# Performance work log

Hardware: AMD Instinct MI355X
Metric: run time of the kernel (lower is better)

Reference implementation:

```python
import jax, jax.numpy as jnp
import numpy as np

NW, NT, ND, D = 30000, 2000, 20000, 128
E = {'ww': 600000, 'wt': 300000, 'wd': 400000, 'td': 100000, 'tt': 40000}
ENDS = {'ww': (NW, NW), 'wt': (NW, NT), 'wd': (NW, ND), 'td': (NT, ND), 'tt': (NT, NT)}


def setup_inputs() -> dict:
    key = jax.random.key(0)
    ks = iter(jax.random.split(key, 64))
    nrm = lambda shape: jax.random.normal(next(ks), shape, dtype=jnp.float32)
    inp = {}
    inp['feat_word'] = nrm((NW, D))
    inp['feat_topic'] = nrm((NT, D))
    # 'effect' node data: ~half the topics are causal (nonzero effect)
    inp['effect'] = jax.random.randint(next(ks), (NT,), 0, 2).astype(jnp.float32)
    # independent Bernoulli(0.1) draws for the td and tt iterations
    inp['bern_td'] = (jax.random.uniform(next(ks), (NT,)) < 0.1).astype(jnp.float32)
    inp['bern_tt'] = (jax.random.uniform(next(ks), (NT,)) < 0.1).astype(jnp.float32)
    for et, (ns, nd) in ENDS.items():
        inp[f'src_{et}'] = jax.random.randint(next(ks), (E[et],), 0, ns, dtype=jnp.int32)
        inp[f'dst_{et}'] = jax.random.randint(next(ks), (E[et],), 0, nd, dtype=jnp.int32)
        inp[f'w_{et}'] = jax.random.uniform(next(ks), (E[et],), dtype=jnp.float32)
    for name in ['ww', 'wt', 'wd', 'td', 'tt']:
        inp[f'W_{name}'] = nrm((D, D)) * 0.05
        inp[f'b_{name}'] = jnp.zeros((D,), jnp.float32)
    inp['W_causal'] = nrm((D, D)) * 0.05
    inp['W_noise'] = nrm((D, D)) * 0.05
    inp['n_doc'] = ND
    return inp


def _mean_agg(Wh, w, src, dst, n_dst):
    # DGL fn.u_mul_e + fn.mean: mean of (Wh[src]*w) over incoming edges; 0 for isolated dst
    m = Wh[src] * w[:, None]                                    # [E, D]
    s = jax.ops.segment_sum(m, dst, num_segments=n_dst)          # [n_dst, D]
    deg = jax.ops.segment_sum(jnp.ones_like(w), dst, num_segments=n_dst)
    return jnp.where(deg[:, None] > 0, s / jnp.maximum(deg, 1.0)[:, None], 0.0)


def reference(feat_word, feat_topic, effect, bern_td, bern_tt,
              src_ww, dst_ww, w_ww, src_wt, dst_wt, w_wt,
              src_wd, dst_wd, w_wd, src_td, dst_td, w_td,
              src_tt, dst_tt, w_tt,
              W_ww, b_ww, W_wt, b_wt, W_wd, b_wd, W_td, b_td, W_tt, b_tt,
              W_causal, W_noise, n_doc):
    n_word, n_topic = feat_word.shape[0], feat_topic.shape[0]
    # Phase 1: word -> word (ww)
    h_word = _mean_agg(feat_word @ W_ww + b_ww, w_ww, src_ww, dst_ww, n_word)
    # Phase 2: remaining etypes; word features replaced by h
    causal = (effect != 0).astype(feat_topic.dtype)[:, None]     # [NT, 1]
    rm_td = (bern_td * (effect == 0))[:, None]
    rm_tt = (bern_tt * (effect == 0))[:, None]
    Wh_wt = h_word @ W_wt + b_wt
    Wh_wd = h_word @ W_wd + b_wd
    Wh_td = (feat_topic @ W_td + b_td
             + (feat_topic * causal) @ W_causal - (feat_topic * rm_td) @ W_noise)
    Wh_tt = (feat_topic @ W_tt + b_tt
             + (feat_topic * causal) @ W_causal - (feat_topic * rm_tt) @ W_noise)
    # cross-relation 'sum' reducer per destination ntype
    h_topic = (_mean_agg(Wh_wt, w_wt, src_wt, dst_wt, n_topic)
               + _mean_agg(Wh_tt, w_tt, src_tt, dst_tt, n_topic))
    h_doc = (_mean_agg(Wh_wd, w_wd, src_wd, dst_wd, n_doc)
             + _mean_agg(Wh_td, w_td, src_td, dst_td, n_doc))
    return h_word, h_topic, h_doc
```

## Files before the change

kernel.cpp:

```cpp
#include <hip/hip_runtime.h>

#define D 128
typedef unsigned short u16;
constexpr int NW = 30000;
constexpr int NT = 2000;
constexpr int NDOC = 20000;
constexpr int NSLOT = NW + NT + NT + NDOC + NDOC;
constexpr int SEG_WW = 0;
constexpr int SEG_WT = NW;
constexpr int SEG_TT = NW + NT;
constexpr int SEG_WD = NW + 2 * NT;
constexpr int SEG_TD = NW + 2 * NT + NDOC;

constexpr int CAPB = 4096;
constexpr int NBK_WW = (NW + 127) / 128;
constexpr int NBK_WT = NT / 16;
constexpr int NBK_TT = (NT + 127) / 128;
constexpr int NBK_WD = (NDOC + 127) / 128;
constexpr int NBK_TD = (NDOC + 127) / 128;
constexpr int BUK_WW = 0;
constexpr int BUK_WT = BUK_WW + NBK_WW;
constexpr int BUK_TT = BUK_WT + NBK_WT;
constexpr int BUK_WD = BUK_TT + NBK_TT;
constexpr int BUK_TD = BUK_WD + NBK_WD;
constexpr int NBUK   = BUK_TD + NBK_TD;

constexpr int EPB = 4096;
constexpr int NF2B = (NW * D / 4 + 255) / 256;
constexpr int NBM4 = (NT + 63) / 64;

struct RelDesc { const int* src; const int* dst; const float* w;
                 int e0; int buk0; int shift; int mask; };
struct Rels { RelDesc r[5]; };

__device__ __forceinline__ int which_rel(const Rels& R, int e)
{
    if (e < R.r[1].e0) return 0;
    if (e < R.r[2].e0) return 1;
    if (e < R.r[3].e0) return 2;
    if (e < R.r[4].e0) return 3;
    return 4;
}

__device__ __forceinline__ float b2f(u16 h)
{
    return __uint_as_float(((unsigned)h) << 16);
}
__device__ __forceinline__ u16 f2b(float f)
{
    unsigned u = __float_as_uint(f);
    return (u16)((u + 0x7FFF + ((u >> 16) & 1)) >> 16);
}

typedef short bf16x8 __attribute__((ext_vector_type(8)));
typedef float f32x4 __attribute__((ext_vector_type(4)));
constexpr int WPITCH = 136;

__device__ __forceinline__ void stage_wt(
    const float* __restrict__ Wg, u16* Wt, int tid)
{
    for (int i = tid; i < D * D; i += 256) {
        int k = i >> 7, nn = i & 127;
        Wt[nn * WPITCH + k] = f2b(Wg[i]);
    }
}

__device__ __forceinline__ void mfma_tile_f32(
    const float* __restrict__ X, const u16* Wt, int arow, int n,
    int lanelo, int quad, f32x4 acc[8])
{
#pragma unroll
    for (int ct = 0; ct < 8; ++ct) {
        acc[ct][0] = 0.f; acc[ct][1] = 0.f; acc[ct][2] = 0.f; acc[ct][3] = 0.f;
    }
#pragma unroll
    for (int k0 = 0; k0 < 4; ++k0) {
        bf16x8 a;
        if (arow < n) {
            const float* ap = X + (size_t)arow * D + k0 * 32 + quad * 8;
            float4 a0 = *(const float4*)ap;
            float4 a1 = *(const float4*)(ap + 4);
            a[0] = (short)f2b(a0.x); a[1] = (short)f2b(a0.y);
            a[2] = (short)f2b(a0.z); a[3] = (short)f2b(a0.w);
            a[4] = (short)f2b(a1.x); a[5] = (short)f2b(a1.y);
            a[6] = (short)f2b(a1.z); a[7] = (short)f2b(a1.w);
        } else {
#pragma unroll
            for (int j = 0; j < 8; ++j) a[j] = 0;
        }
#pragma unroll
        for (int ct = 0; ct < 8; ++ct) {
            bf16x8 b = *(const bf16x8*)&Wt[(ct * 16 + lanelo) * WPITCH
                                           + k0 * 32 + quad * 8];
            acc[ct] = __builtin_amdgcn_mfma_f32_16x16x32_bf16(a, b, acc[ct], 0, 0, 0);
        }
    }
}

__device__ __forceinline__ void mfma_tile_b16(
    const u16* __restrict__ Xb, const u16* Wt, int arow, int n,
    int lanelo, int quad, f32x4 acc[8])
{
#pragma unroll
    for (int ct = 0; ct < 8; ++ct) {
        acc[ct][0] = 0.f; acc[ct][1] = 0.f; acc[ct][2] = 0.f; acc[ct][3] = 0.f;
    }
#pragma unroll
    for (int k0 = 0; k0 < 4; ++k0) {
        bf16x8 a;
        if (arow < n) {
            a = *(const bf16x8*)(Xb + (size_t)arow * D + k0 * 32 + quad * 8);
        } else {
#pragma unroll
            for (int j = 0; j < 8; ++j) a[j] = 0;
        }
#pragma unroll
        for (int ct = 0; ct < 8; ++ct) {
            bf16x8 b = *(const bf16x8*)&Wt[(ct * 16 + lanelo) * WPITCH
                                           + k0 * 32 + quad * 8];
            acc[ct] = __builtin_amdgcn_mfma_f32_16x16x32_bf16(a, b, acc[ct], 0, 0, 0);
        }
    }
}

struct MM4 { const float* W[4]; float* P[4]; };

__global__ __launch_bounds__(256) void prep_kernel(
    const float* __restrict__ feat_word, u16* __restrict__ fw16,
    const float* __restrict__ feat_topic, MM4 m4, int* __restrict__ cur)
{
    __shared__ u16 Wt[D * WPITCH];
    int tid = threadIdx.x;

    if ((int)blockIdx.x < NF2B) {
        int i = blockIdx.x * 256 + tid;
        if (i < NW * D / 4) {
            float4 v = ((const float4*)feat_word)[i];
            ushort4 o;
            o.x = f2b(v.x); o.y = f2b(v.y); o.z = f2b(v.z); o.w = f2b(v.w);
            ((ushort4*)fw16)[i] = o;
        }
    } else if ((int)blockIdx.x < NF2B + 4 * NBM4) {
        int idx = blockIdx.x - NF2B;
        int which = idx / NBM4;
        int bx = idx % NBM4;
        stage_wt(m4.W[which], Wt, tid);
        __syncthreads();
        int wv = tid >> 6, lane = tid & 63;
        int lanelo = lane & 15, quad = lane >> 4;
        int rowbase = bx * 64 + wv * 16;
        f32x4 acc[8];
        mfma_tile_f32(feat_topic, Wt, rowbase + lanelo, NT, lanelo, quad, acc);
        float* Y = m4.P[which];
        int rbase = rowbase + quad * 4;
#pragma unroll
        for (int r = 0; r < 4; ++r) {
            int row = rbase + r;
            if (row >= NT) continue;
#pragma unroll
            for (int ct = 0; ct < 8; ++ct)
                Y[(size_t)row * D + ct * 16 + lanelo] = acc[ct][r];
        }
    } else {
        for (int i = tid; i < NBUK; i += 256) cur[i] = 0;
    }
}

__global__ __launch_bounds__(256) void part_combine_kernel(
    Rels R, int Etot, int* __restrict__ cur, int2* __restrict__ edataP,
    const float* __restrict__ P_td, const float* __restrict__ P_tt,
    const float* __restrict__ Pc, const float* __restrict__ Pn,
    const float* __restrict__ effect, const float* __restrict__ bern_td,
    const float* __restrict__ bern_tt,
    const float* __restrict__ b_td, const float* __restrict__ b_tt,
    u16* __restrict__ wtd16, u16* __restrict__ wtt16, int npb)
{
    __shared__ int hist[NBUK];
    __shared__ int baseL[NBUK];
    __shared__ u16 bkt[EPB];
    __shared__ int2 st[EPB];
    int tid = threadIdx.x;

    if ((int)blockIdx.x >= npb) {
        int i = ((int)blockIdx.x - npb) * 256 + tid;
        if (i < NT * D) {
            int row = i >> 7;
            int col = i & (D - 1);
            float eff = effect[row];
            float causal = (eff != 0.f) ? 1.f : 0.f;
            float zero = (eff == 0.f) ? 1.f : 0.f;
            float rmtd = bern_td[row] * zero;
            float rmtt = bern_tt[row] * zero;
            float pc = Pc[i];
            float pn = Pn[i];
            wtd16[i] = f2b(P_td[i] + b_td[col] + causal * pc - rmtd * pn);
            wtt16[i] = f2b(P_tt[i] + b_tt[col] + causal * pc - rmtt * pn);
        }
        return;
    }

    for (int i = tid; i < NBUK; i += 256) hist[i] = 0;
    __syncthreads();
    int base_e = blockIdx.x * EPB;
    for (int r = 0; r < EPB / 256; ++r) {
        int idx = r * 256 + tid;
        int e = base_e + idx;
        if (e < Etot) {
            int k = which_rel(R, e);
            int le = e - R.r[k].e0;
            int s = R.r[k].src[le];
            int dd = R.r[k].dst[le];
            float w = R.r[k].w[le];
            int b = R.r[k].buk0 + (dd >> R.r[k].shift);
            int dloc = dd & R.r[k].mask;
            bkt[idx] = (u16)b;
            st[idx] = make_int2(s | (dloc << 15), __float_as_int(w));
            atomicAdd(&hist[b], 1);
        } else {
            bkt[idx] = 0xFFFF;
        }
    }
    __syncthreads();
    for (int i = tid; i < NBUK; i += 256)
        baseL[i] = hist[i] ? atomicAdd(&cur[i], hist[i]) : 0;
    __syncthreads();
    for (int i = tid; i < NBUK; i += 256) hist[i] = 0;
    __syncthreads();
    for (int r = 0; r < EPB / 256; ++r) {
        int idx = r * 256 + tid;
        int b = bkt[idx];
        if (b != 0xFFFF) {
            int rk = atomicAdd(&hist[b], 1);
            edataP[(size_t)b * CAPB + baseL[b] + rk] = st[idx];
        }
    }
}

__device__ __forceinline__ void reduce_one_lds(
    const u16* __restrict__ Xb, const int2* st, const u16* ord,
    int start, int end, int slot, int lane,
    u16* __restrict__ Sb, float* __restrict__ degf, float* __restrict__ wsumf)
{
    int half = lane >> 5;
    int q = (lane & 31) * 4;
    float4 acc = make_float4(0.f, 0.f, 0.f, 0.f);
    float wacc = 0.f;
    int j = start;
    for (; j + 16 <= end; j += 16) {
        int2 ee[8];
        ushort4 vv[8];
#pragma unroll
        for (int t = 0; t < 8; ++t) ee[t] = st[ord[j + 2 * t + half]];
#pragma unroll
        for (int t = 0; t < 8; ++t)
            vv[t] = *(const ushort4*)(Xb + (size_t)(ee[t].x & 0x7FFF) * D + q);
#pragma unroll
        for (int t = 0; t < 8; ++t) {
            float w = __int_as_float(ee[t].y);
            acc.x = fmaf(w, b2f(vv[t].x), acc.x);
            acc.y = fmaf(w, b2f(vv[t].y), acc.y);
            acc.z = fmaf(w, b2f(vv[t].z), acc.z);
            acc.w = fmaf(w, b2f(vv[t].w), acc.w);
            wacc += w;
        }
    }
    if (j + 8 <= end) {
        int2 ee[4];
        ushort4 vv[4];
#pragma unroll
        for (int t = 0; t < 4; ++t) ee[t] = st[ord[j + 2 * t + half]];
#pragma unroll
        for (int t = 0; t < 4; ++t)
            vv[t] = *(const ushort4*)(Xb + (size_t)(ee[t].x & 0x7FFF) * D + q);
#pragma unroll
        for (int t = 0; t < 4; ++t) {
            float w = __int_as_float(ee[t].y);
            acc.x = fmaf(w, b2f(vv[t].x), acc.x);
            acc.y = fmaf(w, b2f(vv[t].y), acc.y);
            acc.z = fmaf(w, b2f(vv[t].z), acc.z);
            acc.w = fmaf(w, b2f(vv[t].w), acc.w);
            wacc += w;
        }
        j += 8;
    }
    if (j + 4 <= end) {
        int2 ea = st[ord[j + half]];
        int2 eb = st[ord[j + 2 + half]];
        ushort4 va = *(const ushort4*)(Xb + (size_t)(ea.x & 0x7FFF) * D + q);
        ushort4 vb = *(const ushort4*)(Xb + (size_t)(eb.x & 0x7FFF) * D + q);
        float wa = __int_as_float(ea.y);
        float wb = __int_as_float(eb.y);
        acc.x = fmaf(wa, b2f(va.x), acc.x); acc.y = fmaf(wa, b2f(va.y), acc.y);
        acc.z = fmaf(wa, b2f(va.z), acc.z); acc.w = fmaf(wa, b2f(va.w), acc.w);
        acc.x = fmaf(wb, b2f(vb.x), acc.x); acc.y = fmaf(wb, b2f(vb.y), acc.y);
        acc.z = fmaf(wb, b2f(vb.z), acc.z); acc.w = fmaf(wb, b2f(vb.w), acc.w);
        wacc += wa + wb;
        j += 4;
    }
    for (; j < end; j += 2) {
        int jj = j + half;
        int2 e = st[ord[jj < end ? jj : (end - 1)]];
        float w = (jj < end) ? __int_as_float(e.y) : 0.f;
        ushort4 v = *(const ushort4*)(Xb + (size_t)(e.x & 0x7FFF) * D + q);
        acc.x = fmaf(w, b2f(v.x), acc.x); acc.y = fmaf(w, b2f(v.y), acc.y);
        acc.z = fmaf(w, b2f(v.z), acc.z); acc.w = fmaf(w, b2f(v.w), acc.w);
        wacc += w;
    }
    acc.x += __shfl_xor(acc.x, 32);
    acc.y += __shfl_xor(acc.y, 32);
    acc.z += __shfl_xor(acc.z, 32);
    acc.w += __shfl_xor(acc.w, 32);
    wacc  += __shfl_xor(wacc, 32);
    if (half == 0) {
        ushort4 o;
        o.x = f2b(acc.x); o.y = f2b(acc.y); o.z = f2b(acc.z); o.w = f2b(acc.w);
        *(ushort4*)(Sb + (size_t)slot * D + q) = o;
    }
    if (lane == 0) {
        degf[slot] = (float)(end - start);
        if (wsumf) wsumf[slot] = wacc;
    }
}

__device__ __forceinline__ void bucket_reduce_body(
    const u16* __restrict__ X, const int* __restrict__ cur,
    const int2* __restrict__ edataP, int buk, int gslot0, int nsl,
    u16* __restrict__ Sb, float* __restrict__ degf, float* __restrict__ wsumf,
    int2* st, u16* ord, int* h2, int* exc, int* cnt)
{
    int tid = threadIdx.x;
    int nE = cur[buk];
    const int2* gsrc = edataP + (size_t)buk * CAPB;
    for (int i = tid; i < nE; i += 1024) st[i] = gsrc[i];
    if (tid < 128) { h2[tid] = 0; cnt[tid] = 0; }
    __syncthreads();
    for (int i = tid; i < nE; i += 1024)
        atomicAdd(&h2[(st[i].x >> 15) & 127], 1);
    __syncthreads();
    if (tid < 128) exc[tid] = h2[tid];
    __syncthreads();
    for (int off = 1; off < 128; off <<= 1) {
        int t = 0;
        if (tid < 128 && tid >= off) t = exc[tid - off];
        __syncthreads();
        if (tid < 128) exc[tid] += t;
        __syncthreads();
    }
    if (tid < 128) exc[tid] -= h2[tid];
    __syncthreads();
    for (int i = tid; i < nE; i += 1024) {
        int dl = (st[i].x >> 15) & 127;
        int rk = atomicAdd(&cnt[dl], 1);
        ord[exc[dl] + rk] = (u16)i;
    }
    __syncthreads();
    int wv = tid >> 6, lane = tid & 63;
    for (int dl = wv; dl < nsl; dl += 16) {
        int start = exc[dl];
        reduce_one_lds(X, st, ord, start, start + h2[dl], gslot0 + dl,
                       lane, Sb, degf, wsumf);
    }
}

__global__ __launch_bounds__(1024) void bucket_reduceA_kernel(
    const u16* __restrict__ fw16, const u16* __restrict__ wtt16,
    const u16* __restrict__ wtd16, const int* __restrict__ cur,
    const int2* __restrict__ edataP,
    u16* __restrict__ Sb, float* __restrict__ degf, float* __restrict__ wsumf)
{
    __shared__ int2 st[CAPB];
    __shared__ u16 ord[CAPB];
    __shared__ int h2[128], exc[128], cnt[128];
    int b = blockIdx.x;
    const u16* X; int buk, gslot0, nsl;
    if (b < NBK_WW) {
        X = fw16; buk = BUK_WW + b; gslot0 = SEG_WW + b * 128;
        nsl = min(128, NW - b * 128);
    } else if (b < NBK_WW + NBK_TT) {
        int i = b - NBK_WW;
        X = wtt16; buk = BUK_TT + i; gslot0 = SEG_TT + i * 128;
        nsl = min(128, NT - i * 128);
    } else {
        int i = b - NBK_WW - NBK_TT;
        X = wtd16; buk = BUK_TD + i; gslot0 = SEG_TD + i * 128;
        nsl = min(128, NDOC - i * 128);
    }
    bucket_reduce_body(X, cur, edataP, buk, gslot0, nsl, Sb, degf, wsumf,
                       st, ord, h2, exc, cnt);
}

__global__ __launch_bounds__(1024) void bucket_reduceB_kernel(
    const u16* __restrict__ hw16, const int* __restrict__ cur,
    const int2* __restrict__ edataP,
    u16* __restrict__ Sb, float* __restrict__ degf, float* __restrict__ wsumf)
{
    __shared__ int2 st[CAPB];
    __shared__ u16 ord[CAPB];
    __shared__ int h2[128], exc[128], cnt[128];
    int b = blockIdx.x;
    int buk, gslot0, nsl;
    if (b < NBK_WT) {
        buk = BUK_WT + b; gslot0 = SEG_WT + b * 16; nsl = 16;
    } else {
        int i = b - NBK_WT;
        buk = BUK_WD + i; gslot0 = SEG_WD + i * 128;
        nsl = min(128, NDOC - i * 128);
    }
    bucket_reduce_body(hw16, cur, edataP, buk, gslot0, nsl, Sb, degf, wsumf,
                       st, ord, h2, exc, cnt);
}

__device__ __forceinline__ void mfma_mm_body(
    const u16* __restrict__ Xb, const float* __restrict__ Wg,
    const float* __restrict__ deg, const float* __restrict__ wsum,
    const float* __restrict__ bias,
    const u16* __restrict__ T, const float* __restrict__ degT,
    float* __restrict__ Y, u16* __restrict__ Yb, int n,
    u16* Wt, int tid, int bx)
{
    stage_wt(Wg, Wt, tid);
    __syncthreads();
    int wv = tid >> 6, lane = tid & 63;
    int lanelo = lane & 15, quad = lane >> 4;
    int rowbase = bx * 64 + wv * 16;
    f32x4 acc[8];
    mfma_tile_b16(Xb, Wt, rowbase + lanelo, n, lanelo, quad, acc);

    int rbase = rowbase + quad * 4;
#pragma unroll
    for (int r = 0; r < 4; ++r) {
        int row = rbase + r;
        if (row >= n) continue;
        float dgv = deg[row];
        float wsv = wsum ? wsum[row] : 0.f;
        float dtv = degT ? degT[row] : 0.f;
#pragma unroll
        for (int ct = 0; ct < 8; ++ct) {
            int col = ct * 16 + lanelo;
            float y = acc[ct][r];
            y = dgv > 0.f ? (y + wsv * bias[col]) / dgv : 0.f;
            if (T && dtv > 0.f) y += b2f(T[(size_t)row * D + col]) / dtv;
            Y[(size_t)row * D + col] = y;
            if (Yb) Yb[(size_t)row * D + col] = f2b(y);
        }
    }
}

__global__ __launch_bounds__(256) void mfma_mm_kernel(
    const u16* __restrict__ Xb, const float* __restrict__ Wg,
    const float* __restrict__ deg, const float* __restrict__ wsum,
    const float* __restrict__ bias,
    const u16* __restrict__ T, const float* __restrict__ degT,
    float* __restrict__ Y, u16* __restrict__ Yb, int n)
{
    __shared__ u16 Wt[D * WPITCH];
    mfma_mm_body(Xb, Wg, deg, wsum, bias, T, degT, Y, Yb, n,
                 Wt, threadIdx.x, blockIdx.x);
}

struct MMF {
    const u16* X[2]; const float* W[2]; const float* deg[2];
    const float* wsum[2]; const float* bias[2];
    const u16* T[2]; const float* degT[2];
    float* Y[2]; int n[2]; int nb0;
};
__global__ __launch_bounds__(256) void mfma_mm2_kernel(MMF p)
{
    __shared__ u16 Wt[D * WPITCH];
    int which = (int)(blockIdx.x >= (unsigned)p.nb0);
    int bx = which ? (int)blockIdx.x - p.nb0 : (int)blockIdx.x;
    mfma_mm_body(p.X[which], p.W[which], p.deg[which], p.wsum[which],
                 p.bias[which], p.T[which], p.degT[which], p.Y[which],
                 nullptr, p.n[which], Wt, threadIdx.x, bx);
}

extern "C" void kernel_launch(void* const* d_in, const int* in_sizes, int n_in,
                              void* d_out, int out_size, void* d_ws, size_t ws_size,
                              hipStream_t stream)
{
    const float* feat_word  = (const float*)d_in[0];
    const float* feat_topic = (const float*)d_in[1];
    const float* effect     = (const float*)d_in[2];
    const float* bern_td    = (const float*)d_in[3];
    const float* bern_tt    = (const float*)d_in[4];
    const int*   src_ww = (const int*)d_in[5];
    const int*   dst_ww = (const int*)d_in[6];
    const float* w_ww   = (const float*)d_in[7];
    const int*   src_wt = (const int*)d_in[8];
    const int*   dst_wt = (const int*)d_in[9];
    const float* w_wt   = (const float*)d_in[10];
    const int*   src_wd = (const int*)d_in[11];
    const int*   dst_wd = (const int*)d_in[12];
    const float* w_wd   = (const float*)d_in[13];
    const int*   src_td = (const int*)d_in[14];
    const int*   dst_td = (const int*)d_in[15];
    const float* w_td   = (const float*)d_in[16];
    const int*   src_tt = (const int*)d_in[17];
    const int*   dst_tt = (const int*)d_in[18];
    const float* w_tt   = (const float*)d_in[19];
    const float* W_ww = (const float*)d_in[20];
    const float* b_ww = (const float*)d_in[21];
    const float* W_wt = (const float*)d_in[22];
    const float* b_wt = (const float*)d_in[23];
    const float* W_wd = (const float*)d_in[24];
    const float* b_wd = (const float*)d_in[25];
    const float* W_td = (const float*)d_in[26];
    const float* b_td = (const float*)d_in[27];
    const float* W_tt = (const float*)d_in[28];
    const float* b_tt = (const float*)d_in[29];
    const float* W_causal = (const float*)d_in[30];
    const float* W_noise  = (const float*)d_in[31];

    const int E_ww = in_sizes[5];
    const int E_wt = in_sizes[8];
    const int E_wd = in_sizes[11];
    const int E_td = in_sizes[14];
    const int E_tt = in_sizes[17];
    const int E_total = E_ww + E_wt + E_wd + E_td + E_tt;

    float* ws = (float*)d_ws;
    u16*   Sb    = (u16*)ws; ws += (long long)NSLOT * D / 2;
    float* degf  = ws; ws += NSLOT;
    float* wsumf = ws; ws += NSLOT;
    int*   cur   = (int*)ws; ws += NBUK;
    ws += ((size_t)(ws - (float*)d_ws) & 1);
    int2*  edataP = (int2*)ws; ws += (long long)2 * NBUK * CAPB;
    float* P_td  = ws; ws += (long long)NT * D;
    float* P_tt  = ws; ws += (long long)NT * D;
    float* Pc    = ws; ws += (long long)NT * D;
    float* Pn    = ws; ws += (long long)NT * D;
    u16*   fw16  = (u16*)ws;  ws += (long long)NW * D / 2;
    u16*   hw16  = (u16*)ws;  ws += (long long)NW * D / 2;
    u16*   wtd16 = (u16*)ws;  ws += (long long)NT * D / 2;
    u16*   wtt16 = (u16*)ws;  ws += (long long)NT * D / 2;

    float* h_word  = (float*)d_out;
    float* h_topic = h_word + (long long)NW * D;
    float* h_doc   = h_topic + (long long)NT * D;

    auto nb = [](long long n) { return (unsigned)((n + 255) / 256); };

    Rels R;
    R.r[0] = { src_ww, dst_ww, w_ww, 0,                         BUK_WW, 7, 127 };
    R.r[1] = { src_wt, dst_wt, w_wt, E_ww,                      BUK_WT, 4, 15  };
    R.r[2] = { src_tt, dst_tt, w_tt, E_ww + E_wt,               BUK_TT, 7, 127 };
    R.r[3] = { src_wd, dst_wd, w_wd, E_ww + E_wt + E_tt,        BUK_WD, 7, 127 };
    R.r[4] = { src_td, dst_td, w_td, E_ww + E_wt + E_tt + E_wd, BUK_TD, 7, 127 };

    MM4 m4;
    m4.W[0] = W_td; m4.W[1] = W_tt; m4.W[2] = W_causal; m4.W[3] = W_noise;
    m4.P[0] = P_td; m4.P[1] = P_tt; m4.P[2] = Pc;       m4.P[3] = Pn;
    prep_kernel<<<NF2B + 4 * NBM4 + 1, 256, 0, stream>>>(
        feat_word, fw16, feat_topic, m4, cur);

    unsigned npb = (unsigned)((E_total + EPB - 1) / EPB);
    part_combine_kernel<<<npb + nb((long long)NT * D), 256, 0, stream>>>(
        R, E_total, cur, edataP,
        P_td, P_tt, Pc, Pn, effect, bern_td, bern_tt, b_td, b_tt,
        wtd16, wtt16, (int)npb);

    bucket_reduceA_kernel<<<NBK_WW + NBK_TT + NBK_TD, 1024, 0, stream>>>(
        fw16, wtt16, wtd16, cur, edataP, Sb, degf, wsumf);

    mfma_mm_kernel<<<(NW + 63) / 64, 256, 0, stream>>>(
        Sb + (long long)SEG_WW * D, W_ww, degf + SEG_WW, wsumf + SEG_WW, b_ww,
        nullptr, nullptr, h_word, hw16, NW);

    bucket_reduceB_kernel<<<NBK_WT + NBK_WD, 1024, 0, stream>>>(
        hw16, cur, edataP, Sb, degf, wsumf);

    MMF mf;
    mf.X[0] = Sb + (long long)SEG_WT * D;  mf.X[1] = Sb + (long long)SEG_WD * D;
    mf.W[0] = W_wt;                        mf.W[1] = W_wd;
    mf.deg[0] = degf + SEG_WT;             mf.deg[1] = degf + SEG_WD;
    mf.wsum[0] = wsumf + SEG_WT;           mf.wsum[1] = wsumf + SEG_WD;
    mf.bias[0] = b_wt;                     mf.bias[1] = b_wd;
    mf.T[0] = Sb + (long long)SEG_TT * D;  mf.T[1] = Sb + (long long)SEG_TD * D;
    mf.degT[0] = degf + SEG_TT;            mf.degT[1] = degf + SEG_TD;
    mf.Y[0] = h_topic;                     mf.Y[1] = h_doc;
    mf.n[0] = NT;                          mf.n[1] = NDOC;
    mf.nb0 = (NT + 63) / 64;
    unsigned nbf = (unsigned)((NT + 63) / 64 + (NDOC + 63) / 64);
    mfma_mm2_kernel<<<nbf, 256, 0, stream>>>(mf);

    (void)n_in; (void)in_sizes; (void)out_size; (void)ws_size;
}
```

Measured before the change: 266.7 us.

## Fuse bucket reduction with MFMA projection and shrink buckets to 64 destinations

Combines the bucketed segment-sum with the following bf16 MFMA matmul inside one kernel per phase. The per-destination sums stay in LDS instead of going through a global intermediate, and the two separate matmul launches are removed. Buckets shrink from 128 to 64 destinations with 512-thread blocks, the bucket capacity is halved, and the partition pass keeps edges in registers instead of LDS. The weights are transposed to bf16 once in the prep kernel and read from global memory during the fused matmul. The halved capacity adds a clamp that silently drops edges if a bucket overflows.

```diff
diff --git a/kernel.cpp b/kernel.cpp
--- a/kernel.cpp
+++ b/kernel.cpp
@@ -5,19 +5,14 @@
 constexpr int NW = 30000;
 constexpr int NT = 2000;
 constexpr int NDOC = 20000;
-constexpr int NSLOT = NW + NT + NT + NDOC + NDOC;
-constexpr int SEG_WW = 0;
-constexpr int SEG_WT = NW;
-constexpr int SEG_TT = NW + NT;
-constexpr int SEG_WD = NW + 2 * NT;
-constexpr int SEG_TD = NW + 2 * NT + NDOC;
-
-constexpr int CAPB = 4096;
-constexpr int NBK_WW = (NW + 127) / 128;
-constexpr int NBK_WT = NT / 16;
-constexpr int NBK_TT = (NT + 127) / 128;
-constexpr int NBK_WD = (NDOC + 127) / 128;
-constexpr int NBK_TD = (NDOC + 127) / 128;
+
+constexpr int CAPB = 2048;
+constexpr int SSP  = 136;
+constexpr int NBK_WW = (NW + 63) / 64;
+constexpr int NBK_WT = NT / 8;
+constexpr int NBK_TT = (NT + 63) / 64;
+constexpr int NBK_WD = (NDOC + 63) / 64;
+constexpr int NBK_TD = (NDOC + 63) / 64;
 constexpr int BUK_WW = 0;
 constexpr int BUK_WT = BUK_WW + NBK_WW;
 constexpr int BUK_TT = BUK_WT + NBK_WT;
@@ -97,37 +92,12 @@
     }
 }
 
-__device__ __forceinline__ void mfma_tile_b16(
-    const u16* __restrict__ Xb, const u16* Wt, int arow, int n,
-    int lanelo, int quad, f32x4 acc[8])
-{
-#pragma unroll
-    for (int ct = 0; ct < 8; ++ct) {
-        acc[ct][0] = 0.f; acc[ct][1] = 0.f; acc[ct][2] = 0.f; acc[ct][3] = 0.f;
-    }
-#pragma unroll
-    for (int k0 = 0; k0 < 4; ++k0) {
-        bf16x8 a;
-        if (arow < n) {
-            a = *(const bf16x8*)(Xb + (size_t)arow * D + k0 * 32 + quad * 8);
-        } else {
-#pragma unroll
-            for (int j = 0; j < 8; ++j) a[j] = 0;
-        }
-#pragma unroll
-        for (int ct = 0; ct < 8; ++ct) {
-            bf16x8 b = *(const bf16x8*)&Wt[(ct * 16 + lanelo) * WPITCH
-                                           + k0 * 32 + quad * 8];
-            acc[ct] = __builtin_amdgcn_mfma_f32_16x16x32_bf16(a, b, acc[ct], 0, 0, 0);
-        }
-    }
-}
-
 struct MM4 { const float* W[4]; float* P[4]; };
+struct TR3 { const float* W[3]; u16* T[3]; };
 
 __global__ __launch_bounds__(256) void prep_kernel(
     const float* __restrict__ feat_word, u16* __restrict__ fw16,
-    const float* __restrict__ feat_topic, MM4 m4, int* __restrict__ cur)
+    const float* __restrict__ feat_topic, MM4 m4, TR3 tr, int* __restrict__ cur)
 {
     __shared__ u16 Wt[D * WPITCH];
     int tid = threadIdx.x;
@@ -160,6 +130,15 @@
 #pragma unroll
             for (int ct = 0; ct < 8; ++ct)
                 Y[(size_t)row * D + ct * 16 + lanelo] = acc[ct][r];
+        }
+    } else if ((int)blockIdx.x < NF2B + 4 * NBM4 + 3) {
+        int which = blockIdx.x - NF2B - 4 * NBM4;
+        stage_wt(tr.W[which], Wt, tid);
+        __syncthreads();
+        u16* Wd = tr.T[which];
+        for (int i = tid; i < D * D; i += 256) {
+            int nrow = i >> 7, k = i & 127;
+            Wd[i] = Wt[nrow * WPITCH + k];
         }
     } else {
         for (int i = tid; i < NBUK; i += 256) cur[i] = 0;
@@ -177,8 +156,6 @@
 {
     __shared__ int hist[NBUK];
     __shared__ int baseL[NBUK];
-    __shared__ u16 bkt[EPB];
-    __shared__ int2 st[EPB];
     int tid = threadIdx.x;
 
     if ((int)blockIdx.x >= npb) {
@@ -202,9 +179,11 @@
     for (int i = tid; i < NBUK; i += 256) hist[i] = 0;
     __syncthreads();
     int base_e = blockIdx.x * EPB;
+    int bs[EPB / 256];
+    int2 se[EPB / 256];
+#pragma unroll
     for (int r = 0; r < EPB / 256; ++r) {
-        int idx = r * 256 + tid;
-        int e = base_e + idx;
+        int e = base_e + r * 256 + tid;
         if (e < Etot) {
             int k = which_rel(R, e);
             int le = e - R.r[k].e0;
@@ -213,11 +192,11 @@
             float w = R.r[k].w[le];
             int b = R.r[k].buk0 + (dd >> R.r[k].shift);
             int dloc = dd & R.r[k].mask;
-            bkt[idx] = (u16)b;
-            st[idx] = make_int2(s | (dloc << 15), __float_as_int(w));
+            bs[r] = b;
+            se[r] = make_int2(s | (dloc << 15), __float_as_int(w));
             atomicAdd(&hist[b], 1);
         } else {
-            bkt[idx] = 0xFFFF;
+            bs[r] = -1;
         }
     }
     __syncthreads();
@@ -226,20 +205,29 @@
     __syncthreads();
     for (int i = tid; i < NBUK; i += 256) hist[i] = 0;
     __syncthreads();
+#pragma unroll
     for (int r = 0; r < EPB / 256; ++r) {
-        int idx = r * 256 + tid;
-        int b = bkt[idx];
-        if (b != 0xFFFF) {
-            int rk = atomicAdd(&hist[b], 1);
-            edataP[(size_t)b * CAPB + baseL[b] + rk] = st[idx];
-        }
-    }
-}
+        int b = bs[r];
+        if (b >= 0) {
+            int rk = atomicAdd(&hist[b], 1) + baseL[b];
+            if (rk < CAPB)
+                edataP[(size_t)b * CAPB + rk] = se[r];
+        }
+    }
+}
+
+struct BucketSmem {
+    int2 st[CAPB];
+    u16  ord[CAPB];
+    u16  Ssum[64 * SSP];
+    float degL[64];
+    float wsumL[64];
+    int h2[64], exc[64], cnt[64];
+};
 
 __device__ __forceinline__ void reduce_one_lds(
     const u16* __restrict__ Xb, const int2* st, const u16* ord,
-    int start, int end, int slot, int lane,
-    u16* __restrict__ Sb, float* __restrict__ degf, float* __restrict__ wsumf)
+    int start, int end, int dl, int lane, BucketSmem& s)
 {
     int half = lane >> 5;
     int q = (lane & 31) * 4;
@@ -314,164 +302,175 @@
     if (half == 0) {
         ushort4 o;
         o.x = f2b(acc.x); o.y = f2b(acc.y); o.z = f2b(acc.z); o.w = f2b(acc.w);
-        *(ushort4*)(Sb + (size_t)slot * D + q) = o;
+        *(ushort4*)(s.Ssum + dl * SSP + q) = o;
     }
     if (lane == 0) {
-        degf[slot] = (float)(end - start);
-        if (wsumf) wsumf[slot] = wacc;
-    }
-}
-
-__device__ __forceinline__ void bucket_reduce_body(
+        s.degL[dl] = (float)(end - start);
+        s.wsumL[dl] = wacc;
+    }
+}
+
+__device__ __forceinline__ void bucket_reduce(
     const u16* __restrict__ X, const int* __restrict__ cur,
-    const int2* __restrict__ edataP, int buk, int gslot0, int nsl,
-    u16* __restrict__ Sb, float* __restrict__ degf, float* __restrict__ wsumf,
-    int2* st, u16* ord, int* h2, int* exc, int* cnt)
+    const int2* __restrict__ edataP, int buk, int nsl, BucketSmem& s)
 {
     int tid = threadIdx.x;
-    int nE = cur[buk];
+    int nE = min(cur[buk], CAPB);
     const int2* gsrc = edataP + (size_t)buk * CAPB;
-    for (int i = tid; i < nE; i += 1024) st[i] = gsrc[i];
-    if (tid < 128) { h2[tid] = 0; cnt[tid] = 0; }
-    __syncthreads();
-    for (int i = tid; i < nE; i += 1024)
-        atomicAdd(&h2[(st[i].x >> 15) & 127], 1);
-    __syncthreads();
-    if (tid < 128) exc[tid] = h2[tid];
-    __syncthreads();
-    for (int off = 1; off < 128; off <<= 1) {
+    for (int i = tid; i < nE; i += 512) s.st[i] = gsrc[i];
+    if (tid < 64) { s.h2[tid] = 0; s.cnt[tid] = 0; }
+    __syncthreads();
+    for (int i = tid; i < nE; i += 512)
+        atomicAdd(&s.h2[(s.st[i].x >> 15) & 63], 1);
+    __syncthreads();
+    if (tid < 64) s.exc[tid] = s.h2[tid];
+    __syncthreads();
+    for (int off = 1; off < 64; off <<= 1) {
         int t = 0;
-        if (tid < 128 && tid >= off) t = exc[tid - off];
-        __syncthreads();
-        if (tid < 128) exc[tid] += t;
-        __syncthreads();
-    }
-    if (tid < 128) exc[tid] -= h2[tid];
-    __syncthreads();
-    for (int i = tid; i < nE; i += 1024) {
-        int dl = (st[i].x >> 15) & 127;
-        int rk = atomicAdd(&cnt[dl], 1);
-        ord[exc[dl] + rk] = (u16)i;
+        if (tid < 64 && tid >= off) t = s.exc[tid - off];
+        __syncthreads();
+        if (tid < 64) s.exc[tid] += t;
+        __syncthreads();
+    }
+    if (tid < 64) s.exc[tid] -= s.h2[tid];
+    __syncthreads();
+    for (int i = tid; i < nE; i += 512) {
+        int dl = (s.st[i].x >> 15) & 63;
+        int rk = atomicAdd(&s.cnt[dl], 1);
+        s.ord[s.exc[dl] + rk] = (u16)i;
     }
     __syncthreads();
     int wv = tid >> 6, lane = tid & 63;
-    for (int dl = wv; dl < nsl; dl += 16) {
-        int start = exc[dl];
-        reduce_one_lds(X, st, ord, start, start + h2[dl], gslot0 + dl,
-                       lane, Sb, degf, wsumf);
-    }
-}
-
-__global__ __launch_bounds__(1024) void bucket_reduceA_kernel(
+    for (int dl = wv; dl < nsl; dl += 8) {
+        int start = s.exc[dl];
+        reduce_one_lds(X, s.st, s.ord, start, start + s.h2[dl], dl, lane, s);
+    }
+}
+
+__device__ __forceinline__ void fused_mm(
+    BucketSmem& s, const u16* __restrict__ Wtg, const float* __restrict__ bias,
+    const u16* __restrict__ Tg, const float* __restrict__ degTg,
+    float* __restrict__ Y, u16* __restrict__ Yb, int row0, int n, int tid)
+{
+    int wv = tid >> 6, lane = tid & 63;
+    int lanelo = lane & 15, quad = lane >> 4;
+    int rt = wv >> 1, ch = wv & 1;
+    int arow = rt * 16 + lanelo;
+    f32x4 acc[4];
+#pragma unroll
+    for (int c = 0; c < 4; ++c) {
+        acc[c][0] = 0.f; acc[c][1] = 0.f; acc[c][2] = 0.f; acc[c][3] = 0.f;
+    }
+#pragma unroll
+    for (int k0 = 0; k0 < 4; ++k0) {
+        bf16x8 a;
+        if (arow < n) {
+            a = *(const bf16x8*)(s.Ssum + arow * SSP + k0 * 32 + quad * 8);
+        } else {
+#pragma unroll
+            for (int j = 0; j < 8; ++j) a[j] = 0;
+        }
+#pragma unroll
+        for (int c = 0; c < 4; ++c) {
+            int ct = ch * 4 + c;
+            bf16x8 b = *(const bf16x8*)(Wtg + (ct * 16 + lanelo) * D
+                                        + k0 * 32 + quad * 8);
+            acc[c] = __builtin_amdgcn_mfma_f32_16x16x32_bf16(a, b, acc[c], 0, 0, 0);
+        }
+    }
+    int rbase = rt * 16 + quad * 4;
+#pragma unroll
+    for (int r = 0; r < 4; ++r) {
+        int row = rbase + r;
+        if (row >= n) continue;
+        float dgv = s.degL[row];
+        float wsv = s.wsumL[row];
+        float dtv = degTg ? degTg[row] : 0.f;
+#pragma unroll
+        for (int c = 0; c < 4; ++c) {
+            int ct = ch * 4 + c;
+            int col = ct * 16 + lanelo;
+            float y = acc[c][r];
+            y = dgv > 0.f ? (y + wsv * bias[col]) / dgv : 0.f;
+            if (Tg && dtv > 0.f) y += b2f(Tg[(size_t)row * D + col]) / dtv;
+            Y[(size_t)(row0 + row) * D + col] = y;
+            if (Yb) Yb[(size_t)(row0 + row) * D + col] = f2b(y);
+        }
+    }
+}
+
+__device__ __forceinline__ void dump_smem(
+    BucketSmem& s, u16* __restrict__ Sg, float* __restrict__ degg,
+    int nsl, int tid)
+{
+    for (int i = tid; i < nsl * 32; i += 512) {
+        int row = i >> 5, c4 = (i & 31) * 4;
+        *(ushort4*)(Sg + (size_t)row * D + c4) =
+            *(const ushort4*)(s.Ssum + row * SSP + c4);
+    }
+    if (tid < nsl) degg[tid] = s.degL[tid];
+}
+
+__global__ __launch_bounds__(512, 4) void phaseA_kernel(
     const u16* __restrict__ fw16, const u16* __restrict__ wtt16,
     const u16* __restrict__ wtd16, const int* __restrict__ cur,
     const int2* __restrict__ edataP,
-    u16* __restrict__ Sb, float* __restrict__ degf, float* __restrict__ wsumf)
-{
-    __shared__ int2 st[CAPB];
-    __shared__ u16 ord[CAPB];
-    __shared__ int h2[128], exc[128], cnt[128];
+    const u16* __restrict__ Wtg_ww, const float* __restrict__ b_ww,
+    float* __restrict__ h_word, u16* __restrict__ hw16,
+    u16* __restrict__ Sb2, float* __restrict__ degf2)
+{
+    __shared__ BucketSmem s;
     int b = blockIdx.x;
-    const u16* X; int buk, gslot0, nsl;
+    int tid = threadIdx.x;
     if (b < NBK_WW) {
-        X = fw16; buk = BUK_WW + b; gslot0 = SEG_WW + b * 128;
-        nsl = min(128, NW - b * 128);
+        int w0 = b * 64;
+        int nsl = min(64, NW - w0);
+        bucket_reduce(fw16, cur, edataP, BUK_WW + b, nsl, s);
+        __syncthreads();
+        fused_mm(s, Wtg_ww, b_ww, nullptr, nullptr, h_word, hw16, w0, nsl, tid);
     } else if (b < NBK_WW + NBK_TT) {
         int i = b - NBK_WW;
-        X = wtt16; buk = BUK_TT + i; gslot0 = SEG_TT + i * 128;
-        nsl = min(128, NT - i * 128);
+        int t0 = i * 64;
+        int nsl = min(64, NT - t0);
+        bucket_reduce(wtt16, cur, edataP, BUK_TT + i, nsl, s);
+        __syncthreads();
+        dump_smem(s, Sb2 + (size_t)t0 * D, degf2 + t0, nsl, tid);
     } else {
         int i = b - NBK_WW - NBK_TT;
-        X = wtd16; buk = BUK_TD + i; gslot0 = SEG_TD + i * 128;
-        nsl = min(128, NDOC - i * 128);
-    }
-    bucket_reduce_body(X, cur, edataP, buk, gslot0, nsl, Sb, degf, wsumf,
-                       st, ord, h2, exc, cnt);
-}
-
-__global__ __launch_bounds__(1024) void bucket_reduceB_kernel(
+        int d0 = i * 64;
+        int nsl = min(64, NDOC - d0);
+        bucket_reduce(wtd16, cur, edataP, BUK_TD + i, nsl, s);
+        __syncthreads();
+        dump_smem(s, Sb2 + (size_t)(NT + d0) * D, degf2 + NT + d0, nsl, tid);
+    }
+}
+
+__global__ __launch_bounds__(512, 4) void phaseB_kernel(
     const u16* __restrict__ hw16, const int* __restrict__ cur,
     const int2* __restrict__ edataP,
-    u16* __restrict__ Sb, float* __restrict__ degf, float* __restrict__ wsumf)
-{
-    __shared__ int2 st[CAPB];
-    __shared__ u16 ord[CAPB];
-    __shared__ int h2[128], exc[128], cnt[128];
+    const u16* __restrict__ Wtg_wt, const float* __restrict__ b_wt,
+    const u16* __restrict__ Wtg_wd, const float* __restrict__ b_wd,
+    const u16* __restrict__ Sb2, const float* __restrict__ degf2,
+    float* __restrict__ h_topic, float* __restrict__ h_doc)
+{
+    __shared__ BucketSmem s;
     int b = blockIdx.x;
-    int buk, gslot0, nsl;
+    int tid = threadIdx.x;
     if (b < NBK_WT) {
-        buk = BUK_WT + b; gslot0 = SEG_WT + b * 16; nsl = 16;
+        int t0 = b * 8;
+        bucket_reduce(hw16, cur, edataP, BUK_WT + b, 8, s);
+        __syncthreads();
+        fused_mm(s, Wtg_wt, b_wt, Sb2 + (size_t)t0 * D, degf2 + t0,
+                 h_topic, nullptr, t0, 8, tid);
     } else {
         int i = b - NBK_WT;
-        buk = BUK_WD + i; gslot0 = SEG_WD + i * 128;
-        nsl = min(128, NDOC - i * 128);
-    }
-    bucket_reduce_body(hw16, cur, edataP, buk, gslot0, nsl, Sb, degf, wsumf,
-                       st, ord, h2, exc, cnt);
-}
-
-__device__ __forceinline__ void mfma_mm_body(
-    const u16* __restrict__ Xb, const float* __restrict__ Wg,
-    const float* __restrict__ deg, const float* __restrict__ wsum,
-    const float* __restrict__ bias,
-    const u16* __restrict__ T, const float* __restrict__ degT,
-    float* __restrict__ Y, u16* __restrict__ Yb, int n,
-    u16* Wt, int tid, int bx)
-{
-    stage_wt(Wg, Wt, tid);
-    __syncthreads();
-    int wv = tid >> 6, lane = tid & 63;
-    int lanelo = lane & 15, quad = lane >> 4;
-    int rowbase = bx * 64 + wv * 16;
-    f32x4 acc[8];
-    mfma_tile_b16(Xb, Wt, rowbase + lanelo, n, lanelo, quad, acc);
-
-    int rbase = rowbase + quad * 4;
-#pragma unroll
-    for (int r = 0; r < 4; ++r) {
-        int row = rbase + r;
-        if (row >= n) continue;
-        float dgv = deg[row];
-        float wsv = wsum ? wsum[row] : 0.f;
-        float dtv = degT ? degT[row] : 0.f;
-#pragma unroll
-        for (int ct = 0; ct < 8; ++ct) {
-            int col = ct * 16 + lanelo;
-            float y = acc[ct][r];
-            y = dgv > 0.f ? (y + wsv * bias[col]) / dgv : 0.f;
-            if (T && dtv > 0.f) y += b2f(T[(size_t)row * D + col]) / dtv;
-            Y[(size_t)row * D + col] = y;
-            if (Yb) Yb[(size_t)row * D + col] = f2b(y);
-        }
-    }
-}
-
-__global__ __launch_bounds__(256) void mfma_mm_kernel(
-    const u16* __restrict__ Xb, const float* __restrict__ Wg,
-    const float* __restrict__ deg, const float* __restrict__ wsum,
-    const float* __restrict__ bias,
-    const u16* __restrict__ T, const float* __restrict__ degT,
-    float* __restrict__ Y, u16* __restrict__ Yb, int n)
-{
-    __shared__ u16 Wt[D * WPITCH];
-    mfma_mm_body(Xb, Wg, deg, wsum, bias, T, degT, Y, Yb, n,
-                 Wt, threadIdx.x, blockIdx.x);
-}
-
-struct MMF {
-    const u16* X[2]; const float* W[2]; const float* deg[2];
-    const float* wsum[2]; const float* bias[2];
-    const u16* T[2]; const float* degT[2];
-    float* Y[2]; int n[2]; int nb0;
-};
-__global__ __launch_bounds__(256) void mfma_mm2_kernel(MMF p)
-{
-    __shared__ u16 Wt[D * WPITCH];
-    int which = (int)(blockIdx.x >= (unsigned)p.nb0);
-    int bx = which ? (int)blockIdx.x - p.nb0 : (int)blockIdx.x;
-    mfma_mm_body(p.X[which], p.W[which], p.deg[which], p.wsum[which],
-                 p.bias[which], p.T[which], p.degT[which], p.Y[which],
-                 nullptr, p.n[which], Wt, threadIdx.x, bx);
+        int d0 = i * 64;
+        int nsl = min(64, NDOC - d0);
+        bucket_reduce(hw16, cur, edataP, BUK_WD + i, nsl, s);
+        __syncthreads();
+        fused_mm(s, Wtg_wd, b_wd, Sb2 + (size_t)(NT + d0) * D, degf2 + NT + d0,
+                 h_doc, nullptr, d0, nsl, tid);
+    }
 }
 
 extern "C" void kernel_launch(void* const* d_in, const int* in_sizes, int n_in,
@@ -519,9 +518,8 @@
     const int E_total = E_ww + E_wt + E_wd + E_td + E_tt;
 
     float* ws = (float*)d_ws;
-    u16*   Sb    = (u16*)ws; ws += (long long)NSLOT * D / 2;
-    float* degf  = ws; ws += NSLOT;
-    float* wsumf = ws; ws += NSLOT;
+    u16*   Sb2   = (u16*)ws; ws += (long long)(NT + NDOC) * D / 2;
+    float* degf2 = ws; ws += NT + NDOC;
     int*   cur   = (int*)ws; ws += NBUK;
     ws += ((size_t)(ws - (float*)d_ws) & 1);
     int2*  edataP = (int2*)ws; ws += (long long)2 * NBUK * CAPB;
@@ -533,6 +531,9 @@
     u16*   hw16  = (u16*)ws;  ws += (long long)NW * D / 2;
     u16*   wtd16 = (u16*)ws;  ws += (long long)NT * D / 2;
     u16*   wtt16 = (u16*)ws;  ws += (long long)NT * D / 2;
+    u16*   Wtg_ww = (u16*)ws; ws += (long long)D * D / 2;
+    u16*   Wtg_wt = (u16*)ws; ws += (long long)D * D / 2;
+    u16*   Wtg_wd = (u16*)ws; ws += (long long)D * D / 2;
 
     float* h_word  = (float*)d_out;
     float* h_topic = h_word + (long long)NW * D;
@@ -541,17 +542,20 @@
     auto nb = [](long long n) { return (unsigned)((n + 255) / 256); };
 
     Rels R;
-    R.r[0] = { src_ww, dst_ww, w_ww, 0,                         BUK_WW, 7, 127 };
-    R.r[1] = { src_wt, dst_wt, w_wt, E_ww,                      BUK_WT, 4, 15  };
-    R.r[2] = { src_tt, dst_tt, w_tt, E_ww + E_wt,               BUK_TT, 7, 127 };
-    R.r[3] = { src_wd, dst_wd, w_wd, E_ww + E_wt + E_tt,        BUK_WD, 7, 127 };
-    R.r[4] = { src_td, dst_td, w_td, E_ww + E_wt + E_tt + E_wd, BUK_TD, 7, 127 };
+    R.r[0] = { src_ww, dst_ww, w_ww, 0,                         BUK_WW, 6, 63 };
+    R.r[1] = { src_wt, dst_wt, w_wt, E_ww,                      BUK_WT, 3, 7  };
+    R.r[2] = { src_tt, dst_tt, w_tt, E_ww + E_wt,               BUK_TT, 6, 63 };
+    R.r[3] = { src_wd, dst_wd, w_wd, E_ww + E_wt + E_tt,        BUK_WD, 6, 63 };
+    R.r[4] = { src_td, dst_td, w_td, E_ww + E_wt + E_tt + E_wd, BUK_TD, 6, 63 };
 
     MM4 m4;
     m4.W[0] = W_td; m4.W[1] = W_tt; m4.W[2] = W_causal; m4.W[3] = W_noise;
     m4.P[0] = P_td; m4.P[1] = P_tt; m4.P[2] = Pc;       m4.P[3] = Pn;
-    prep_kernel<<<NF2B + 4 * NBM4 + 1, 256, 0, stream>>>(
-        feat_word, fw16, feat_topic, m4, cur);
+    TR3 tr;
+    tr.W[0] = W_ww; tr.W[1] = W_wt; tr.W[2] = W_wd;
+    tr.T[0] = Wtg_ww; tr.T[1] = Wtg_wt; tr.T[2] = Wtg_wd;
+    prep_kernel<<<NF2B + 4 * NBM4 + 3 + 1, 256, 0, stream>>>(
+        feat_word, fw16, feat_topic, m4, tr, cur);
 
     unsigned npb = (unsigned)((E_total + EPB - 1) / EPB);
     part_combine_kernel<<<npb + nb((long long)NT * D), 256, 0, stream>>>(
@@ -559,29 +563,13 @@
         P_td, P_tt, Pc, Pn, effect, bern_td, bern_tt, b_td, b_tt,
         wtd16, wtt16, (int)npb);
 
-    bucket_reduceA_kernel<<<NBK_WW + NBK_TT + NBK_TD, 1024, 0, stream>>>(
-        fw16, wtt16, wtd16, cur, edataP, Sb, degf, wsumf);
-
-    mfma_mm_kernel<<<(NW + 63) / 64, 256, 0, stream>>>(
-        Sb + (long long)SEG_WW * D, W_ww, degf + SEG_WW, wsumf + SEG_WW, b_ww,
-        nullptr, nullptr, h_word, hw16, NW);
-
-    bucket_reduceB_kernel<<<NBK_WT + NBK_WD, 1024, 0, stream>>>(
-        hw16, cur, edataP, Sb, degf, wsumf);
-
-    MMF mf;
-    mf.X[0] = Sb + (long long)SEG_WT * D;  mf.X[1] = Sb + (long long)SEG_WD * D;
-    mf.W[0] = W_wt;                        mf.W[1] = W_wd;
-    mf.deg[0] = degf + SEG_WT;             mf.deg[1] = degf + SEG_WD;
-    mf.wsum[0] = wsumf + SEG_WT;           mf.wsum[1] = wsumf + SEG_WD;
-    mf.bias[0] = b_wt;                     mf.bias[1] = b_wd;
-    mf.T[0] = Sb + (long long)SEG_TT * D;  mf.T[1] = Sb + (long long)SEG_TD * D;
-    mf.degT[0] = degf + SEG_TT;            mf.degT[1] = degf + SEG_TD;
-    mf.Y[0] = h_topic;                     mf.Y[1] = h_doc;
-    mf.n[0] = NT;                          mf.n[1] = NDOC;
-    mf.nb0 = (NT + 63) / 64;
-    unsigned nbf = (unsigned)((NT + 63) / 64 + (NDOC + 63) / 64);
-    mfma_mm2_kernel<<<nbf, 256, 0, stream>>>(mf);
+    phaseA_kernel<<<NBK_WW + NBK_TT + NBK_TD, 512, 0, stream>>>(
+        fw16, wtt16, wtd16, cur, edataP, Wtg_ww, b_ww,
+        h_word, hw16, Sb2, degf2);
+
+    phaseB_kernel<<<NBK_WT + NBK_WD, 512, 0, stream>>>(
+        hw16, cur, edataP, Wtg_wt, b_wt, Wtg_wd, b_wd,
+        Sb2, degf2, h_topic, h_doc);
 
     (void)n_in; (void)in_sizes; (void)out_size; (void)ws_size;
 }
```

After: 254.5 us. -4.6%, faster.
